# Kernel optimization log

Measured on AMD Instinct MI355X. Metric: run time of the kernel, lower is better.

Reference implementation:

```python
import jax, jax.numpy as jnp
import numpy as np

D_MODEL = 512
H = 8
D_K = D_MODEL // H
NEG = -1.0e9


def setup_inputs() -> dict:
    key = jax.random.key(0)
    ks = jax.random.split(key, 8)
    B, S = 2, 4096
    q = jax.random.normal(ks[0], (B, S, D_MODEL), dtype=jnp.float32)
    k = jax.random.normal(ks[1], (B, S, D_MODEL), dtype=jnp.float32)
    v = jax.random.normal(ks[2], (B, S, D_MODEL), dtype=jnp.float32)
    mask = jax.random.randint(ks[3], (B, 1, 1, S), 0, 2, dtype=jnp.int32)
    scale = 1.0 / np.sqrt(D_MODEL)
    w_q = jax.random.normal(ks[4], (D_MODEL, D_MODEL), dtype=jnp.float32) * scale
    w_k = jax.random.normal(ks[5], (D_MODEL, D_MODEL), dtype=jnp.float32) * scale
    w_v = jax.random.normal(ks[6], (D_MODEL, D_MODEL), dtype=jnp.float32) * scale
    w_o = jax.random.normal(ks[7], (D_MODEL, D_MODEL), dtype=jnp.float32) * scale
    return {"q": q, "k": k, "v": v, "mask": mask,
            "w_q": w_q, "w_k": w_k, "w_v": w_v, "w_o": w_o}


def reference(q, k, v, mask, w_q, w_k, w_v, w_o):
    B, S, _ = q.shape
    # nn.Linear(x) = x @ W.T; project and split heads -> [B, H, S, D_K]
    def split_heads(x, w):
        return (x @ w.T).reshape(B, -1, H, D_K).transpose(0, 2, 1, 3)
    query = split_heads(q, w_q)
    key_ = split_heads(k, w_k)
    value = split_heads(v, w_v)
    scores = jnp.einsum("bhqd,bhkd->bhqk", query, key_) / jnp.sqrt(
        jnp.asarray(D_K, dtype=q.dtype))
    scores = jnp.where(mask == 0, jnp.asarray(NEG, dtype=scores.dtype), scores)
    attn = jax.nn.softmax(scores, axis=-1)  # dropout p=0.0 (eval)
    x = jnp.einsum("bhqk,bhkd->bhqd", attn, value)
    x = x.transpose(0, 2, 1, 3).reshape(B, S, H * D_K)
    return x @ w_o.T
```

## Files before the change

### kernel.cpp

```cpp
#include <hip/hip_runtime.h>

typedef unsigned short u16;
typedef unsigned int u32;
typedef __attribute__((ext_vector_type(8))) short bf16x8;
typedef __attribute__((ext_vector_type(4))) float f32x4;
typedef __attribute__((ext_vector_type(2))) unsigned int u32x2;

__device__ __forceinline__ u16 f2bf(float f) {
  u32 u = __builtin_bit_cast(u32, f);
  u += 0x7fffu + ((u >> 16) & 1u);
  return (u16)(u >> 16);
}
__device__ __forceinline__ u32 pack2(float a, float b) {
  return (u32)f2bf(a) | ((u32)f2bf(b) << 16);
}

__device__ __forceinline__ void gload_lds16(const u16* g, u16* l) {
  __builtin_amdgcn_global_load_lds(
      (const __attribute__((address_space(1))) void*)g,
      (__attribute__((address_space(3))) void*)l, 16, 0, 0);
}

__global__ __launch_bounds__(256) void cvt3(
    const float* __restrict__ q, const float* __restrict__ k,
    const float* __restrict__ v, u16* __restrict__ dst) {
  int z = blockIdx.y;
  const float* src = (z == 0) ? q : (z == 1) ? k : v;
  int i = blockIdx.x * 256 + threadIdx.x;
  f32x4 f = reinterpret_cast<const f32x4*>(src)[i];
  u32x2 o; o.x = pack2(f[0], f[1]); o.y = pack2(f[2], f[3]);
  reinterpret_cast<u32x2*>(dst + (size_t)z * 4194304)[i] = o;
}

__global__ __launch_bounds__(256) void wm_cvt(
    const float* __restrict__ wq, const float* __restrict__ wk,
    const float* __restrict__ wv, const float* __restrict__ wo,
    const int* __restrict__ mask, u16* __restrict__ Wb, float* __restrict__ madd) {
  int blk = blockIdx.x;
  if (blk < 1024) {
    int z = blk >> 8;
    const float* w = (z == 0) ? wq : (z == 1) ? wk : (z == 2) ? wv : wo;
    int i = (blk & 255) * 256 + threadIdx.x;
    f32x4 f = reinterpret_cast<const f32x4*>(w)[i];
    u32x2 o; o.x = pack2(f[0], f[1]); o.y = pack2(f[2], f[3]);
    reinterpret_cast<u32x2*>(Wb + (size_t)z * 262144)[i] = o;
  } else {
    int i = (blk - 1024) * 256 + threadIdx.x;
    madd[i] = mask[i] ? 0.0f : -2.0e9f;
  }
}

#define BM 128
#define BN 128
#define LDP 40

__device__ __forceinline__ void gemm_core(
    const u16* __restrict__ A, const u16* __restrict__ W,
    int mtile, int ntile, u16* lds_a, u16* lds_b,
    f32x4 acc[4][4], int tid)
{
  int lane = tid & 63;
  int w = tid >> 6;
  int wm = w >> 1, wn = w & 1;
  int ar = tid >> 2;
  int ac = (tid & 3) * 8;
  int lrow = lane & 15, lk = lane >> 4;

  for (int k0 = 0; k0 < 512; k0 += 32) {
    __syncthreads();
#pragma unroll
    for (int rr = 0; rr < BM; rr += 64) {
      int4 va = *reinterpret_cast<const int4*>(A + (mtile + ar + rr) * 512 + k0 + ac);
      *reinterpret_cast<int4*>(lds_a + (ar + rr) * LDP + ac) = va;
      int4 vb = *reinterpret_cast<const int4*>(W + (ntile + ar + rr) * 512 + k0 + ac);
      *reinterpret_cast<int4*>(lds_b + (ar + rr) * LDP + ac) = vb;
    }
    __syncthreads();
    bf16x8 af[4], bfr[4];
#pragma unroll
    for (int i = 0; i < 4; i++) {
      af[i]  = *reinterpret_cast<bf16x8*>(lds_a + (wm * 64 + i * 16 + lrow) * LDP + lk * 8);
      bfr[i] = *reinterpret_cast<bf16x8*>(lds_b + (wn * 64 + i * 16 + lrow) * LDP + lk * 8);
    }
#pragma unroll
    for (int i = 0; i < 4; i++)
#pragma unroll
      for (int j = 0; j < 4; j++)
        acc[i][j] = __builtin_amdgcn_mfma_f32_16x16x32_bf16(af[i], bfr[j], acc[i][j], 0, 0, 0);
  }
}

__global__ __launch_bounds__(256) void proj_gemm(
    const u16* __restrict__ Xb, const u16* __restrict__ Wb,
    u16* __restrict__ Qb, u16* __restrict__ Kb, u16* __restrict__ Vt)
{
  __shared__ u16 lds_a[BM * LDP];
  __shared__ u16 lds_b[BN * LDP];
  int z = blockIdx.z;
  const u16* A = Xb + (size_t)z * (8192 * 512);
  const u16* W = Wb + (size_t)z * (512 * 512);
  f32x4 acc[4][4] = {};
  int mtile = blockIdx.x * BM, ntile = blockIdx.y * BN;
  gemm_core(A, W, mtile, ntile, lds_a, lds_b, acc, threadIdx.x);

  int lane = threadIdx.x & 63;
  int w = threadIdx.x >> 6;
  int wm = w >> 1, wn = w & 1;
  int lrow = lane & 15, lk = lane >> 4;
  u16* dst = (z == 0) ? Qb : (z == 1) ? Kb : Vt;
  float scl = (z == 0) ? 0.18033688011112042f : 1.0f;
#pragma unroll
  for (int i = 0; i < 4; i++)
#pragma unroll
    for (int j = 0; j < 4; j++)
#pragma unroll
      for (int r = 0; r < 4; r++) {
        int m = mtile + wm * 64 + i * 16 + lk * 4 + r;
        int n = ntile + wn * 64 + j * 16 + lrow;
        u16 bv = f2bf(acc[i][j][r] * scl);
        int b = m >> 12, s = m & 4095;
        int h = n >> 6, d = n & 63;
        if (z <= 1) dst[(((size_t)(b * 8 + h) * 4096 + s) * 64 + d)] = bv;
        else        dst[(((size_t)(b * 8 + h) * 64 + d) * 4096 + s)] = bv;
      }
}

__global__ __launch_bounds__(256) void out_gemm(
    const u16* __restrict__ AO, const u16* __restrict__ Wo, float* __restrict__ out)
{
  __shared__ u16 lds_a[BM * LDP];
  __shared__ u16 lds_b[BN * LDP];
  f32x4 acc[4][4] = {};
  int mtile = blockIdx.x * BM, ntile = blockIdx.y * BN;
  gemm_core(AO, Wo, mtile, ntile, lds_a, lds_b, acc, threadIdx.x);

  int lane = threadIdx.x & 63;
  int w = threadIdx.x >> 6;
  int wm = w >> 1, wn = w & 1;
  int lrow = lane & 15, lk = lane >> 4;
#pragma unroll
  for (int i = 0; i < 4; i++)
#pragma unroll
    for (int j = 0; j < 4; j++)
#pragma unroll
      for (int r = 0; r < 4; r++) {
        int m = mtile + wm * 64 + i * 16 + lk * 4 + r;
        int n = ntile + wn * 64 + j * 16 + lrow;
        out[(size_t)m * 512 + n] = acc[i][j][r];
      }
}

__global__ __launch_bounds__(512, 4) void attn_kernel(
    const u16* __restrict__ Qb, const u16* __restrict__ Kb,
    const u16* __restrict__ Vt, const float* __restrict__ madd,
    u16* __restrict__ AO)
{
  __shared__ u16 Kl[2][4096];
  __shared__ u16 Vl[2][4096];
  __shared__ u16 Pl[8][1024];
  int tid = threadIdx.x;
  int lane = tid & 63;
  int w = tid >> 6;
  int lrow = lane & 15, lk = lane >> 4;

  int lb = blockIdx.x;
  int bh = (lb & 7) * 2 + ((lb >> 3) & 1);
  int qt = lb >> 4;
  int b = bh >> 3, h = bh & 7;
  int q0 = qt * 128;

  const u16* Qp = Qb + ((size_t)bh * 4096 + q0 + w * 16 + lrow) * 64;
  bf16x8 bq0 = *(const bf16x8*)(Qp + lk * 8);
  bf16x8 bq1 = *(const bf16x8*)(Qp + 32 + lk * 8);

  const u16* Kbase = Kb + (size_t)bh * (4096 * 64);
  const u16* Vbase = Vt + (size_t)bh * (64 * 4096);
  const float* mq = madd + b * 4096 + lk * 4;

  int trow = w * 8 + (lane >> 3);
  int tch  = (lane & 7) ^ (trow & 7);
  const u16* ksrc = Kbase + (size_t)trow * 64   + tch * 8;
  const u16* vsrc = Vbase + (size_t)trow * 4096 + tch * 8;
  u16* kdst = &Kl[0][0] + w * 512;
  u16* vdst = &Vl[0][0] + w * 512;

  int kc0 = (lk ^ (lrow & 7)) << 4;
  const char* kb0 = (const char*)&Kl[0][0] + lrow * 128 + kc0;
  const char* kb1 = (const char*)&Kl[0][0] + lrow * 128 + (kc0 ^ 64);
  const char* vb0 = (const char*)&Vl[0][0] + lrow * 128 + kc0;
  const char* vb1 = (const char*)&Vl[0][0] + lrow * 128 + (kc0 ^ 64);
  char* pw = (char*)(&Pl[w][0]);
  int pswz = (lrow & 7) << 4;
  char* pwa0 = pw + ((lrow * 128 +  0 + lk * 8) ^ pswz);
  char* pwa1 = pw + ((lrow * 128 + 32 + lk * 8) ^ pswz);
  char* pwa2 = pw + ((lrow * 128 + 64 + lk * 8) ^ pswz);
  char* pwa3 = pw + ((lrow * 128 + 96 + lk * 8) ^ pswz);
  const char* prd0 = pw + ((lrow * 128 +      lk * 16) ^ pswz);
  const char* prd1 = pw + ((lrow * 128 + 64 + lk * 16) ^ pswz);

  float m_r = -3.0e38f;
  f32x4 o[4] = {};
  f32x4 ol = {};
  bf16x8 ones;
#pragma unroll
  for (int i = 0; i < 8; i++) ones[i] = (short)0x3F80;

  gload_lds16(ksrc, kdst);
  gload_lds16(vsrc, vdst);
  __syncthreads();

#define AITER(P, KT)                                                             \
  {                                                                              \
    if ((KT) + 64 < 4096) {                                                      \
      gload_lds16(ksrc + (size_t)((KT) + 64) * 64, kdst + ((P) ^ 1) * 4096);     \
      gload_lds16(vsrc + ((KT) + 64),              vdst + ((P) ^ 1) * 4096);     \
    }                                                                            \
    f32x4 sc[4];                                                                 \
    __builtin_amdgcn_s_setprio(1);                                               \
    _Pragma("unroll")                                                            \
    for (int cb = 0; cb < 4; cb++) {                                             \
      bf16x8 ak0 = *(const bf16x8*)(kb0 + (P) * 8192 + cb * 2048);               \
      bf16x8 ak1 = *(const bf16x8*)(kb1 + (P) * 8192 + cb * 2048);               \
      f32x4 t = {};                                                              \
      t = __builtin_amdgcn_mfma_f32_16x16x32_bf16(ak0, bq0, t, 0, 0, 0);         \
      t = __builtin_amdgcn_mfma_f32_16x16x32_bf16(ak1, bq1, t, 0, 0, 0);         \
      sc[cb] = t;                                                                \
    }                                                                            \
    __builtin_amdgcn_s_setprio(0);                                               \
    _Pragma("unroll")                                                            \
    for (int cb = 0; cb < 4; cb++)                                               \
      sc[cb] += *(const f32x4*)(mq + (KT) + cb * 16);                            \
    float x0 = fmaxf(fmaxf(sc[0][0], sc[0][1]), fmaxf(sc[0][2], sc[0][3]));      \
    float x1 = fmaxf(fmaxf(sc[1][0], sc[1][1]), fmaxf(sc[1][2], sc[1][3]));      \
    float x2 = fmaxf(fmaxf(sc[2][0], sc[2][1]), fmaxf(sc[2][2], sc[2][3]));      \
    float x3 = fmaxf(fmaxf(sc[3][0], sc[3][1]), fmaxf(sc[3][2], sc[3][3]));      \
    float vmax = fmaxf(fmaxf(x0, x1), fmaxf(x2, x3));                            \
    vmax = fmaxf(vmax, __shfl_xor(vmax, 16));                                    \
    vmax = fmaxf(vmax, __shfl_xor(vmax, 32));                                    \
    if (__any(vmax > m_r + 8.0f)) {                                              \
      float mnew = fmaxf(m_r, vmax);                                             \
      float fac = __builtin_amdgcn_exp2f(m_r - mnew);                            \
      o[0] *= fac; o[1] *= fac; o[2] *= fac; o[3] *= fac; ol *= fac;             \
      m_r = mnew;                                                                \
    }                                                                            \
    _Pragma("unroll")                                                            \
    for (int cb = 0; cb < 4; cb++) {                                             \
      float p0 = __builtin_amdgcn_exp2f(sc[cb][0] - m_r);                        \
      float p1 = __builtin_amdgcn_exp2f(sc[cb][1] - m_r);                        \
      float p2 = __builtin_amdgcn_exp2f(sc[cb][2] - m_r);                        \
      float p3 = __builtin_amdgcn_exp2f(sc[cb][3] - m_r);                        \
      u32x2 pk; pk.x = pack2(p0, p1); pk.y = pack2(p2, p3);                      \
      *(u32x2*)(cb == 0 ? pwa0 : cb == 1 ? pwa1 : cb == 2 ? pwa2 : pwa3) = pk;   \
    }                                                                            \
    asm volatile("s_waitcnt lgkmcnt(0)" ::: "memory");                           \
    __builtin_amdgcn_sched_barrier(0);                                           \
    bf16x8 pb0 = *(const bf16x8*)prd0;                                           \
    bf16x8 pb1 = *(const bf16x8*)prd1;                                           \
    __builtin_amdgcn_s_setprio(1);                                               \
    _Pragma("unroll")                                                            \
    for (int nb = 0; nb < 4; nb++) {                                             \
      bf16x8 av0 = *(const bf16x8*)(vb0 + (P) * 8192 + nb * 2048);               \
      bf16x8 av1 = *(const bf16x8*)(vb1 + (P) * 8192 + nb * 2048);               \
      o[nb] = __builtin_amdgcn_mfma_f32_16x16x32_bf16(av0, pb0, o[nb], 0, 0, 0); \
      o[nb] = __builtin_amdgcn_mfma_f32_16x16x32_bf16(av1, pb1, o[nb], 0, 0, 0); \
    }                                                                            \
    ol = __builtin_amdgcn_mfma_f32_16x16x32_bf16(ones, pb0, ol, 0, 0, 0);        \
    ol = __builtin_amdgcn_mfma_f32_16x16x32_bf16(ones, pb1, ol, 0, 0, 0);        \
    __builtin_amdgcn_s_setprio(0);                                               \
    __syncthreads();                                                             \
  }

  for (int kt = 0; kt < 4096; kt += 128) {
    AITER(0, kt)
    AITER(1, kt + 64)
  }
#undef AITER

  float inv = 1.0f / ol[0];
  int srow = q0 + w * 16 + lrow;
#pragma unroll
  for (int nb = 0; nb < 4; nb++) {
    u32x2 pk;
    pk.x = pack2(o[nb][0] * inv, o[nb][1] * inv);
    pk.y = pack2(o[nb][2] * inv, o[nb][3] * inv);
    *(u32x2*)(AO + (size_t)(b * 4096 + srow) * 512 + h * 64 + nb * 16 + lk * 4) = pk;
  }
}

extern "C" void kernel_launch(void* const* d_in, const int* in_sizes, int n_in,
                              void* d_out, int out_size, void* d_ws, size_t ws_size,
                              hipStream_t stream) {
  const float* q  = (const float*)d_in[0];
  const float* k  = (const float*)d_in[1];
  const float* v  = (const float*)d_in[2];
  const int* mask = (const int*)d_in[3];
  const float* wq = (const float*)d_in[4];
  const float* wk = (const float*)d_in[5];
  const float* wv = (const float*)d_in[6];
  const float* wo = (const float*)d_in[7];
  float* out = (float*)d_out;

  u16* ws = (u16*)d_ws;
  u16* Xb = ws;
  u16* Wb = Xb + (size_t)3 * 4194304;
  u16* Qb = Wb + (size_t)4 * 262144;
  u16* Kb = Qb + 4194304;
  u16* Vt = Kb + 4194304;
  u16* AO = Vt + 4194304;
  float* madd = (float*)(AO + 4194304);

  cvt3<<<dim3(4096, 3), 256, 0, stream>>>(q, k, v, Xb);
  wm_cvt<<<1056, 256, 0, stream>>>(wq, wk, wv, wo, mask, Wb, madd);
  proj_gemm<<<dim3(64, 4, 3), 256, 0, stream>>>(Xb, Wb, Qb, Kb, Vt);
  attn_kernel<<<512, 512, 0, stream>>>(Qb, Kb, Vt, madd, AO);
  out_gemm<<<dim3(64, 4), 256, 0, stream>>>(AO, Wb + 3 * 262144, out);
}
```

Measured before the change: 172.9 us.

## Fuse fp32-to-bf16 input conversion into projection GEMM and use cheaper rounding

Drops the separate cvt3 kernel. The projection GEMM now reads the fp32 q/k/v directly and converts them to bf16 while staging into LDS, which removes one launch and a full write-and-reread of the bf16 copies. It also replaces round-to-nearest-even packing with a cheaper round-half-up pack in the attention softmax and output paths, and reorders the max reduction. The cost is twice the global read bytes for the A operand inside the GEMM's k-loop, since each A tile is read once per N tile (4 times), plus slightly different rounding.

```diff
diff --git a/kernel.cpp b/kernel.cpp
--- a/kernel.cpp
+++ b/kernel.cpp
@@ -14,22 +14,16 @@
 __device__ __forceinline__ u32 pack2(float a, float b) {
   return (u32)f2bf(a) | ((u32)f2bf(b) << 16);
 }
+__device__ __forceinline__ u32 pack2_rhu(float a, float b) {
+  u32 ua = __builtin_bit_cast(u32, a) + 0x8000u;
+  u32 ub = __builtin_bit_cast(u32, b) + 0x8000u;
+  return (ua >> 16) | (ub & 0xffff0000u);
+}
 
 __device__ __forceinline__ void gload_lds16(const u16* g, u16* l) {
   __builtin_amdgcn_global_load_lds(
       (const __attribute__((address_space(1))) void*)g,
       (__attribute__((address_space(3))) void*)l, 16, 0, 0);
-}
-
-__global__ __launch_bounds__(256) void cvt3(
-    const float* __restrict__ q, const float* __restrict__ k,
-    const float* __restrict__ v, u16* __restrict__ dst) {
-  int z = blockIdx.y;
-  const float* src = (z == 0) ? q : (z == 1) ? k : v;
-  int i = blockIdx.x * 256 + threadIdx.x;
-  f32x4 f = reinterpret_cast<const f32x4*>(src)[i];
-  u32x2 o; o.x = pack2(f[0], f[1]); o.y = pack2(f[2], f[3]);
-  reinterpret_cast<u32x2*>(dst + (size_t)z * 4194304)[i] = o;
 }
 
 __global__ __launch_bounds__(256) void wm_cvt(
@@ -54,11 +48,20 @@
 #define BN 128
 #define LDP 40
 
-__device__ __forceinline__ void gemm_core(
-    const u16* __restrict__ A, const u16* __restrict__ W,
-    int mtile, int ntile, u16* lds_a, u16* lds_b,
-    f32x4 acc[4][4], int tid)
+__global__ __launch_bounds__(256) void proj_gemm(
+    const float* __restrict__ qf, const float* __restrict__ kf,
+    const float* __restrict__ vf, const u16* __restrict__ Wb,
+    u16* __restrict__ Qb, u16* __restrict__ Kb, u16* __restrict__ Vt)
 {
+  __shared__ u16 lds_a[BM * LDP];
+  __shared__ u16 lds_b[BN * LDP];
+  int z = blockIdx.z;
+  const float* A = (z == 0) ? qf : (z == 1) ? kf : vf;
+  const u16* W = Wb + (size_t)z * 262144;
+  f32x4 acc[4][4] = {};
+  int mtile = blockIdx.x * BM, ntile = blockIdx.y * BN;
+
+  int tid = threadIdx.x;
   int lane = tid & 63;
   int w = tid >> 6;
   int wm = w >> 1, wn = w & 1;
@@ -70,7 +73,12 @@
     __syncthreads();
 #pragma unroll
     for (int rr = 0; rr < BM; rr += 64) {
-      int4 va = *reinterpret_cast<const int4*>(A + (mtile + ar + rr) * 512 + k0 + ac);
+      const float* ap = A + (size_t)(mtile + ar + rr) * 512 + k0 + ac;
+      f32x4 a0 = *reinterpret_cast<const f32x4*>(ap);
+      f32x4 a1 = *reinterpret_cast<const f32x4*>(ap + 4);
+      u32 q0 = pack2_rhu(a0[0], a0[1]), q1 = pack2_rhu(a0[2], a0[3]);
+      u32 q2 = pack2_rhu(a1[0], a1[1]), q3 = pack2_rhu(a1[2], a1[3]);
+      int4 va; va.x = (int)q0; va.y = (int)q1; va.z = (int)q2; va.w = (int)q3;
       *reinterpret_cast<int4*>(lds_a + (ar + rr) * LDP + ac) = va;
       int4 vb = *reinterpret_cast<const int4*>(W + (ntile + ar + rr) * 512 + k0 + ac);
       *reinterpret_cast<int4*>(lds_b + (ar + rr) * LDP + ac) = vb;
@@ -88,25 +96,7 @@
       for (int j = 0; j < 4; j++)
         acc[i][j] = __builtin_amdgcn_mfma_f32_16x16x32_bf16(af[i], bfr[j], acc[i][j], 0, 0, 0);
   }
-}
-
-__global__ __launch_bounds__(256) void proj_gemm(
-    const u16* __restrict__ Xb, const u16* __restrict__ Wb,
-    u16* __restrict__ Qb, u16* __restrict__ Kb, u16* __restrict__ Vt)
-{
-  __shared__ u16 lds_a[BM * LDP];
-  __shared__ u16 lds_b[BN * LDP];
-  int z = blockIdx.z;
-  const u16* A = Xb + (size_t)z * (8192 * 512);
-  const u16* W = Wb + (size_t)z * (512 * 512);
-  f32x4 acc[4][4] = {};
-  int mtile = blockIdx.x * BM, ntile = blockIdx.y * BN;
-  gemm_core(A, W, mtile, ntile, lds_a, lds_b, acc, threadIdx.x);
-
-  int lane = threadIdx.x & 63;
-  int w = threadIdx.x >> 6;
-  int wm = w >> 1, wn = w & 1;
-  int lrow = lane & 15, lk = lane >> 4;
+
   u16* dst = (z == 0) ? Qb : (z == 1) ? Kb : Vt;
   float scl = (z == 0) ? 0.18033688011112042f : 1.0f;
 #pragma unroll
@@ -132,12 +122,38 @@
   __shared__ u16 lds_b[BN * LDP];
   f32x4 acc[4][4] = {};
   int mtile = blockIdx.x * BM, ntile = blockIdx.y * BN;
-  gemm_core(AO, Wo, mtile, ntile, lds_a, lds_b, acc, threadIdx.x);
-
-  int lane = threadIdx.x & 63;
-  int w = threadIdx.x >> 6;
+
+  int tid = threadIdx.x;
+  int lane = tid & 63;
+  int w = tid >> 6;
   int wm = w >> 1, wn = w & 1;
+  int ar = tid >> 2;
+  int ac = (tid & 3) * 8;
   int lrow = lane & 15, lk = lane >> 4;
+
+  for (int k0 = 0; k0 < 512; k0 += 32) {
+    __syncthreads();
+#pragma unroll
+    for (int rr = 0; rr < BM; rr += 64) {
+      int4 va = *reinterpret_cast<const int4*>(AO + (size_t)(mtile + ar + rr) * 512 + k0 + ac);
+      *reinterpret_cast<int4*>(lds_a + (ar + rr) * LDP + ac) = va;
+      int4 vb = *reinterpret_cast<const int4*>(Wo + (size_t)(ntile + ar + rr) * 512 + k0 + ac);
+      *reinterpret_cast<int4*>(lds_b + (ar + rr) * LDP + ac) = vb;
+    }
+    __syncthreads();
+    bf16x8 af[4], bfr[4];
+#pragma unroll
+    for (int i = 0; i < 4; i++) {
+      af[i]  = *reinterpret_cast<bf16x8*>(lds_a + (wm * 64 + i * 16 + lrow) * LDP + lk * 8);
+      bfr[i] = *reinterpret_cast<bf16x8*>(lds_b + (wn * 64 + i * 16 + lrow) * LDP + lk * 8);
+    }
+#pragma unroll
+    for (int i = 0; i < 4; i++)
+#pragma unroll
+      for (int j = 0; j < 4; j++)
+        acc[i][j] = __builtin_amdgcn_mfma_f32_16x16x32_bf16(af[i], bfr[j], acc[i][j], 0, 0, 0);
+  }
+
 #pragma unroll
   for (int i = 0; i < 4; i++)
 #pragma unroll
@@ -230,11 +246,12 @@
     _Pragma("unroll")                                                            \
     for (int cb = 0; cb < 4; cb++)                                               \
       sc[cb] += *(const f32x4*)(mq + (KT) + cb * 16);                            \
-    float x0 = fmaxf(fmaxf(sc[0][0], sc[0][1]), fmaxf(sc[0][2], sc[0][3]));      \
-    float x1 = fmaxf(fmaxf(sc[1][0], sc[1][1]), fmaxf(sc[1][2], sc[1][3]));      \
-    float x2 = fmaxf(fmaxf(sc[2][0], sc[2][1]), fmaxf(sc[2][2], sc[2][3]));      \
-    float x3 = fmaxf(fmaxf(sc[3][0], sc[3][1]), fmaxf(sc[3][2], sc[3][3]));      \
-    float vmax = fmaxf(fmaxf(x0, x1), fmaxf(x2, x3));                            \
+                                           \
+    float x0 = fmaxf(fmaxf(fmaxf(sc[0][0], sc[0][1]), sc[0][2]), sc[0][3]);      \
+    float x1 = fmaxf(fmaxf(fmaxf(sc[1][0], sc[1][1]), sc[1][2]), sc[1][3]);      \
+    float x2 = fmaxf(fmaxf(fmaxf(sc[2][0], sc[2][1]), sc[2][2]), sc[2][3]);      \
+    float x3 = fmaxf(fmaxf(fmaxf(sc[3][0], sc[3][1]), sc[3][2]), sc[3][3]);      \
+    float vmax = fmaxf(fmaxf(fmaxf(x0, x1), x2), x3);                            \
     vmax = fmaxf(vmax, __shfl_xor(vmax, 16));                                    \
     vmax = fmaxf(vmax, __shfl_xor(vmax, 32));                                    \
     if (__any(vmax > m_r + 8.0f)) {                                              \
@@ -249,7 +266,7 @@
       float p1 = __builtin_amdgcn_exp2f(sc[cb][1] - m_r);                        \
       float p2 = __builtin_amdgcn_exp2f(sc[cb][2] - m_r);                        \
       float p3 = __builtin_amdgcn_exp2f(sc[cb][3] - m_r);                        \
-      u32x2 pk; pk.x = pack2(p0, p1); pk.y = pack2(p2, p3);                      \
+      u32x2 pk; pk.x = pack2_rhu(p0, p1); pk.y = pack2_rhu(p2, p3);              \
       *(u32x2*)(cb == 0 ? pwa0 : cb == 1 ? pwa1 : cb == 2 ? pwa2 : pwa3) = pk;   \
     }                                                                            \
     asm volatile("s_waitcnt lgkmcnt(0)" ::: "memory");                           \
@@ -281,8 +298,8 @@
 #pragma unroll
   for (int nb = 0; nb < 4; nb++) {
     u32x2 pk;
-    pk.x = pack2(o[nb][0] * inv, o[nb][1] * inv);
-    pk.y = pack2(o[nb][2] * inv, o[nb][3] * inv);
+    pk.x = pack2_rhu(o[nb][0] * inv, o[nb][1] * inv);
+    pk.y = pack2_rhu(o[nb][2] * inv, o[nb][3] * inv);
     *(u32x2*)(AO + (size_t)(b * 4096 + srow) * 512 + h * 64 + nb * 16 + lk * 4) = pk;
   }
 }
@@ -301,17 +318,15 @@
   float* out = (float*)d_out;
 
   u16* ws = (u16*)d_ws;
-  u16* Xb = ws;
-  u16* Wb = Xb + (size_t)3 * 4194304;
+  u16* Wb = ws;
   u16* Qb = Wb + (size_t)4 * 262144;
   u16* Kb = Qb + 4194304;
   u16* Vt = Kb + 4194304;
   u16* AO = Vt + 4194304;
   float* madd = (float*)(AO + 4194304);
 
-  cvt3<<<dim3(4096, 3), 256, 0, stream>>>(q, k, v, Xb);
   wm_cvt<<<1056, 256, 0, stream>>>(wq, wk, wv, wo, mask, Wb, madd);
-  proj_gemm<<<dim3(64, 4, 3), 256, 0, stream>>>(Xb, Wb, Qb, Kb, Vt);
+  proj_gemm<<<dim3(64, 4, 3), 256, 0, stream>>>(q, k, v, Wb, Qb, Kb, Vt);
   attn_kernel<<<512, 512, 0, stream>>>(Qb, Kb, Vt, madd, AO);
   out_gemm<<<dim3(64, 4), 256, 0, stream>>>(AO, Wb + 3 * 262144, out);
 }
```

New measurement: 162.4 us. 6.1% less time.
